# Performance work log

Measured on AMD Instinct MI355X. Metric: run time of the kernel, lower is better.

The kernel has to match this reference:

```python
import jax, jax.numpy as jnp
import numpy as np

N = 50000; IN_DIM = 128; HID = 128; T = 4; R = 3; E = 500000

def setup_inputs() -> dict:
    key = jax.random.key(0)
    ks = jax.random.split(key, 20)
    def nrm(k, shape, s):
        return jax.random.normal(k, shape, jnp.float32) * s
    s_in = 1.0 / float(np.sqrt(IN_DIM)); s_h = 1.0 / float(np.sqrt(HID))
    return {
        'feat_seq': nrm(ks[0], (T, N, IN_DIM), 1.0),
        'src': jax.random.randint(ks[1], (T, R, E), 0, N, jnp.int32),
        'dst': jax.random.randint(ks[2], (T, R, E), 0, N, jnp.int32),
        'ew': jax.random.uniform(ks[3], (T, R, E), jnp.float32),
        'W_in': nrm(ks[4], (IN_DIM, HID), s_in), 'b_in': jnp.zeros((HID,), jnp.float32),
        'W1': nrm(ks[5], (R, HID, HID), s_h), 'b1': jnp.zeros((R, HID), jnp.float32),
        'W2': nrm(ks[6], (R, HID, HID), s_h), 'b2': jnp.zeros((R, HID), jnp.float32),
        'q1': nrm(ks[7], (HID,), 1.0), 'q2': nrm(ks[8], (HID,), 1.0),
        'ln1_g': jnp.ones((HID,), jnp.float32), 'ln1_b': jnp.zeros((HID,), jnp.float32),
        'ln2_g': jnp.ones((HID,), jnp.float32), 'ln2_b': jnp.zeros((HID,), jnp.float32),
        'gWih': nrm(ks[9], (HID, 3 * HID), s_h), 'gbih': jnp.zeros((3 * HID,), jnp.float32),
        'gWhh': nrm(ks[10], (HID, 3 * HID), s_h), 'gbhh': jnp.zeros((3 * HID,), jnp.float32),
        'temp_q': nrm(ks[11], (HID,), 1.0),
        'tW1': nrm(ks[12], (IN_DIM, HID), s_in), 'tb1': jnp.zeros((HID,), jnp.float32),
        'tW2': nrm(ks[13], (HID, HID), s_h), 'tb2': jnp.zeros((HID,), jnp.float32),
        'cW1': nrm(ks[14], (3 * HID, HID), 1.0 / float(np.sqrt(3 * HID))), 'cb1': jnp.zeros((HID,), jnp.float32),
        'cW2': nrm(ks[15], (HID, 1), s_h), 'cb2': jnp.zeros((1,), jnp.float32),
    }

def _ln(x, g, b):
    m = x.mean(-1, keepdims=True)
    v = ((x - m) ** 2).mean(-1, keepdims=True)
    return (x - m) * jax.lax.rsqrt(v + 1e-5) * g + b

def _rel_attn(stack, q):
    # stack: [R,N,H]; tanh-softmax attention over relations
    score = jnp.einsum('rnh,h->rn', jnp.tanh(stack), q)
    alpha = jax.nn.softmax(score, axis=0)
    return jnp.einsum('rn,rnh->nh', alpha, stack)

def _conv(x, s, d, w, Wr, br):
    # DGL GraphConv norm='right' with edge_weight: mean-by-in-degree weighted SpMM
    msg = w[:, None] * x[s]                                   # [E,H]
    agg = jax.ops.segment_sum(msg, d, num_segments=N)
    deg = jax.ops.segment_sum(jnp.ones_like(w), d, num_segments=N)
    return (agg / jnp.maximum(deg, 1.0)[:, None]) @ Wr + br

def reference(feat_seq, src, dst, ew, W_in, b_in, W1, b1, W2, b2, q1, q2, ln1_g, ln1_b, ln2_g, ln2_b, gWih, gbih, gWhh, gbhh, temp_q, tW1, tb1, tW2, tb2, cW1, cb1, cW2, cb2):
    conv_all = jax.vmap(_conv, in_axes=(None, 0, 0, 0, 0, 0))
    def spatial(x, s, d, w):
        h0 = jax.nn.relu(x @ W_in + b_in)
        h1 = _ln(h0 + jax.nn.relu(_rel_attn(conv_all(h0, s, d, w, W1, b1), q1)), ln1_g, ln1_b)
        h2 = _ln(h1 + jax.nn.relu(_rel_attn(conv_all(h1, s, d, w, W2, b2), q2)), ln2_g, ln2_b)
        return h2
    hs = jnp.stack([spatial(feat_seq[t], src[t], dst[t], ew[t]) for t in range(T)], axis=0)  # [T,N,H]
    def gru_step(h, x):
        gi = x @ gWih + gbih
        gh = h @ gWhh + gbhh
        ir, iz, inn = jnp.split(gi, 3, axis=-1)
        hr, hz, hn = jnp.split(gh, 3, axis=-1)
        r = jax.nn.sigmoid(ir + hr)
        zg = jax.nn.sigmoid(iz + hz)
        n = jnp.tanh(inn + r * hn)
        hnew = (1.0 - zg) * n + zg * h
        return hnew, hnew
    _, outs = jax.lax.scan(gru_step, jnp.zeros((N, HID), feat_seq.dtype), hs)  # [T,N,H]
    out = jnp.transpose(outs, (1, 0, 2))                       # [N,T,H]
    last = out[:, -1, :]
    t_score = jnp.einsum('nth,h->nt', jnp.tanh(out), temp_q)
    t_alpha = jax.nn.softmax(t_score, axis=1)
    attn = jnp.einsum('nt,nth->nh', t_alpha, out)
    tab = jax.nn.relu(jax.nn.relu(feat_seq[-1] @ tW1 + tb1) @ tW2 + tb2)
    z = jnp.concatenate([last, attn, tab], axis=-1)
    return (jax.nn.relu(z @ cW1 + cb1) @ cW2 + cb2)[:, 0]       # [N]
```

## Files before the change

### kernel.cpp

```cpp
#include <hip/hip_runtime.h>
#include <hip/hip_bf16.h>
#include <math.h>

#define NN 50000
#define TT 4
#define RR 3
#define EE 500000
#define RANGE 6400
#define NRANGE 8

typedef __attribute__((ext_vector_type(8))) short bf16x8;
typedef __attribute__((ext_vector_type(4))) float f32x4;

__device__ inline unsigned short f2b(float f)
{
    union { __hip_bfloat16 h; unsigned short u; } cv;
    cv.h = __float2bfloat16(f);
    return cv.u;
}
__device__ inline float b2f(unsigned short u)
{
    union { unsigned int u; float f; } cv;
    cv.u = ((unsigned int)u) << 16;
    return cv.f;
}
__device__ inline bf16x8 pack8(float4 a, float4 b)
{
    bf16x8 r;
    r[0] = (short)f2b(a.x); r[1] = (short)f2b(a.y); r[2] = (short)f2b(a.z); r[3] = (short)f2b(a.w);
    r[4] = (short)f2b(b.x); r[5] = (short)f2b(b.y); r[6] = (short)f2b(b.z); r[7] = (short)f2b(b.w);
    return r;
}


__global__ __launch_bounds__(256)
void diag_kernel(float* __restrict__ out, float v)
{
    int i = blockIdx.x * 256 + threadIdx.x;
    if (i < NN) out[i] = v;
}


__global__ __launch_bounds__(256)
void wswz_kernel(const float* __restrict__ W, unsigned short* __restrict__ dst, int C, int S)
{
    int idx = blockIdx.x * 256 + threadIdx.x;
    int per = 128 * C;
    if (idx >= S * per) return;
    int s = idx / per, rem = idx - s * per;
    int j = rem & 7;
    int lane = (rem >> 3) & 63;
    int blk = rem >> 9;
    int ncg = C >> 4;
    int kc = blk / ncg, cg = blk - kc * ncg;
    int k = kc * 32 + (lane >> 4) * 8 + j;
    int c = cg * 16 + (lane & 15);
    dst[idx] = f2b(W[(size_t)s * 128 * C + (size_t)k * C + c]);
}


__global__ __launch_bounds__(1024)
void count_hist(const int* __restrict__ dst, int* __restrict__ cnt)
{
    __shared__ int hist[RANGE];
    const int g = blockIdx.y;
    const int r0 = blockIdx.x * RANGE;
    for (int i = threadIdx.x; i < RANGE; i += 1024) hist[i] = 0;
    __syncthreads();
    const int4* d4 = (const int4*)(dst + (size_t)g * EE);
    for (int i = threadIdx.x; i < EE / 4; i += 1024) {
        int4 v = d4[i];
        int a0 = v.x - r0; if ((unsigned)a0 < (unsigned)RANGE) atomicAdd(&hist[a0], 1);
        int a1 = v.y - r0; if ((unsigned)a1 < (unsigned)RANGE) atomicAdd(&hist[a1], 1);
        int a2 = v.z - r0; if ((unsigned)a2 < (unsigned)RANGE) atomicAdd(&hist[a2], 1);
        int a3 = v.w - r0; if ((unsigned)a3 < (unsigned)RANGE) atomicAdd(&hist[a3], 1);
    }
    __syncthreads();
    int* c = cnt + (size_t)g * NN;
    for (int i = threadIdx.x; i < RANGE; i += 1024) {
        int n = r0 + i;
        if (n < NN) c[n] = hist[i];
    }
}

__global__ __launch_bounds__(1024)
void scan_kernel(int* __restrict__ cnt, int* __restrict__ rows)
{
    int g = blockIdx.x;
    int tid = threadIdx.x;
    const int CH = (NN + 1023) / 1024;
    int s0 = tid * CH;
    int s1 = s0 + CH; if (s1 > NN) s1 = NN;
    int* c = cnt + (size_t)g * NN;
    int* ro = rows + (size_t)g * (NN + 1);
    int sum = 0;
    for (int i = s0; i < s1; ++i) sum += c[i];
    __shared__ int sd[1024];
    sd[tid] = sum;
    __syncthreads();
    for (int off = 1; off < 1024; off <<= 1) {
        int v = 0;
        if (tid >= off) v = sd[tid - off];
        __syncthreads();
        sd[tid] += v;
        __syncthreads();
    }
    int total = sd[1023];
    int prefix = (tid == 0) ? 0 : sd[tid - 1];
    for (int i = s0; i < s1; ++i) {
        int cv = c[i];
        ro[i] = prefix;
        c[i] = prefix;
        prefix += cv;
    }
    if (tid == 0) ro[NN] = total;
}

__global__ __launch_bounds__(256)
void fill_kernel(const int* __restrict__ src, const int* __restrict__ dst,
                 const float* __restrict__ ew, int* __restrict__ cur,
                 int2* __restrict__ srcw)
{
    int g = blockIdx.y;
    int e = blockIdx.x * 256 + threadIdx.x;
    if (e >= EE) return;
    size_t idx = (size_t)g * EE + e;
    int d = dst[idx];
    int pos = atomicAdd(&cur[(size_t)g * NN + d], 1);
    int2 p;
    p.x = src[idx];
    p.y = __float_as_int(ew[idx]);
    srcw[(size_t)g * EE + pos] = p;
}


__global__ __launch_bounds__(256)
void agg16_kernel(const unsigned short* __restrict__ x16,
                  const int2* __restrict__ srcw,
                  const int* __restrict__ rows,
                  unsigned short* __restrict__ agg16)
{
    int wid = (blockIdx.x * 256 + threadIdx.x) >> 6;
    int lane = threadIdx.x & 63;
    if (wid >= RR * NN) return;
    int r = wid / NN;
    int n = wid - r * NN;
    const int* rs = rows + (size_t)r * (NN + 1);
    int e0 = rs[n], e1 = rs[n + 1];
    const int2* sw = srcw + (size_t)r * EE;
    const int co = lane * 2;
    float ax = 0.f, ay = 0.f;
    for (int e = e0; e < e1; e += 16) {
        int2 p[16];
        unsigned int v[16];
#pragma unroll
        for (int i = 0; i < 16; ++i) {
            int idx = (e + i < e1) ? e + i : e1 - 1;
            p[i] = sw[idx];
        }
#pragma unroll
        for (int i = 0; i < 16; ++i)
            v[i] = *(const unsigned int*)(x16 + (size_t)p[i].x * 128 + co);
#pragma unroll
        for (int i = 0; i < 16; ++i) {
            float w = (e + i < e1) ? __int_as_float(p[i].y) : 0.f;
            ax += w * b2f((unsigned short)(v[i] & 0xffffu));
            ay += w * b2f((unsigned short)(v[i] >> 16));
        }
    }
    float inv = 1.0f / fmaxf((float)(e1 - e0), 1.0f);
    unsigned int o = (unsigned int)f2b(ax * inv) | ((unsigned int)f2b(ay * inv) << 16);
    *(unsigned int*)(agg16 + ((size_t)r * NN + n) * 128 + co) = o;
}


__global__ __launch_bounds__(256)
void mmb(const void* in, int in_bf16, long in_zs, int ldin,
         const unsigned short* __restrict__ Ws, long w_zs,
         const float* __restrict__ bias, long b_zs,
         float* out, long out_zs, int ldout,
         unsigned short* out16, long out16_zs,
         int rows, int act)
{
    const int tid = threadIdx.x;
    const int wv = tid >> 6, l = tid & 63;
    const int z = blockIdx.z;
    const int r0 = blockIdx.x * 64 + wv * 16;
    const int lk = (l >> 4) * 8;
    int rowA = r0 + (l & 15);
    int rowc = rowA < rows ? rowA : rows - 1;

    bf16x8 a[4];
    if (in_bf16) {
        const unsigned short* inb = (const unsigned short*)in + (size_t)z * in_zs
                                    + (size_t)rowc * ldin + lk;
#pragma unroll
        for (int kc = 0; kc < 4; ++kc) {
            uint4 u = *(const uint4*)(inb + kc * 32);
            a[kc] = *(bf16x8*)&u;
        }
    } else {
        const float* inf = (const float*)in + (size_t)z * in_zs
                           + (size_t)rowc * ldin + lk;
#pragma unroll
        for (int kc = 0; kc < 4; ++kc) {
            float4 u0 = *(const float4*)(inf + kc * 32);
            float4 u1 = *(const float4*)(inf + kc * 32 + 4);
            a[kc] = pack8(u0, u1);
        }
    }

    const unsigned short* Wz = Ws + (size_t)z * w_zs;
    const float* bz = bias + (size_t)z * b_zs;
    float* oz = out ? out + (size_t)z * out_zs : (float*)0;
    unsigned short* o16z = out16 ? out16 + (size_t)z * out16_zs : (unsigned short*)0;
    const int colbase = l & 15;
    const int rbase = r0 + (l >> 4) * 4;

#pragma unroll
    for (int cg = 0; cg < 8; ++cg) {
        f32x4 acc = {0.f, 0.f, 0.f, 0.f};
#pragma unroll
        for (int kc = 0; kc < 4; ++kc) {
            uint4 bu = *(const uint4*)(Wz + ((size_t)(kc * 8 + cg) * 64 + l) * 8);
            acc = __builtin_amdgcn_mfma_f32_16x16x32_bf16(a[kc], *(bf16x8*)&bu, acc, 0, 0, 0);
        }
        int col = cg * 16 + colbase;
        float bvv = bz[col];
#pragma unroll
        for (int j = 0; j < 4; ++j) {
            int gr = rbase + j;
            if (gr >= rows) continue;
            float v = acc[j] + bvv;
            if (act) v = fmaxf(v, 0.f);
            if (oz) oz[(size_t)gr * ldout + col] = v;
            if (o16z) o16z[(size_t)gr * 128 + col] = f2b(v);
        }
    }
}


__global__ __launch_bounds__(256)
void grub4(float* HS,
           const unsigned short* __restrict__ Wis, const float* __restrict__ bi,
           const unsigned short* __restrict__ Whs, const float* __restrict__ bh)
{
    __shared__ __align__(16) unsigned short hbuf[4][16 * 136];
    const int tid = threadIdx.x;
    const int wv = tid >> 6, l = tid & 63;
    const int r0 = blockIdx.x * 64 + wv * 16;
    const int lo = l & 15, hi = l >> 4;
    const int lk = hi * 8;
    const int rowc = (r0 + lo) < NN ? (r0 + lo) : NN - 1;
    const int rbase = r0 + hi * 4;
    unsigned short* hb = hbuf[wv];

    for (int i = l; i < 16 * 136; i += 64) hb[i] = 0;

    float hold[8][4];
#pragma unroll
    for (int cg = 0; cg < 8; ++cg)
#pragma unroll
        for (int j = 0; j < 4; ++j) hold[cg][j] = 0.f;

#pragma unroll 1
    for (int t = 0; t < TT; ++t) {
        float* xt = HS + (size_t)t * NN * 128;
        bf16x8 ax[4], hx[4];
        const float* bx = xt + (size_t)rowc * 128 + lk;
#pragma unroll
        for (int kc = 0; kc < 4; ++kc) {
            ax[kc] = pack8(*(const float4*)(bx + kc * 32), *(const float4*)(bx + kc * 32 + 4));
            uint4 hu = *(const uint4*)(hb + lo * 136 + kc * 32 + lk);
            hx[kc] = *(bf16x8*)&hu;
        }

#pragma unroll 1
        for (int cg = 0; cg < 8; ++cg) {
            f32x4 air = {0.f,0.f,0.f,0.f}, ahr = {0.f,0.f,0.f,0.f};
            f32x4 aiz = {0.f,0.f,0.f,0.f}, ahz = {0.f,0.f,0.f,0.f};
            f32x4 ain = {0.f,0.f,0.f,0.f}, ahn = {0.f,0.f,0.f,0.f};
#pragma unroll
            for (int kc = 0; kc < 4; ++kc) {
                uint4 br = *(const uint4*)(Wis + ((size_t)(kc * 24 + 0 + cg) * 64 + l) * 8);
                uint4 hr = *(const uint4*)(Whs + ((size_t)(kc * 24 + 0 + cg) * 64 + l) * 8);
                uint4 bz = *(const uint4*)(Wis + ((size_t)(kc * 24 + 8 + cg) * 64 + l) * 8);
                uint4 hz = *(const uint4*)(Whs + ((size_t)(kc * 24 + 8 + cg) * 64 + l) * 8);
                uint4 bn = *(const uint4*)(Wis + ((size_t)(kc * 24 + 16 + cg) * 64 + l) * 8);
                uint4 hn = *(const uint4*)(Whs + ((size_t)(kc * 24 + 16 + cg) * 64 + l) * 8);
                air = __builtin_amdgcn_mfma_f32_16x16x32_bf16(ax[kc], *(bf16x8*)&br, air, 0, 0, 0);
                ahr = __builtin_amdgcn_mfma_f32_16x16x32_bf16(hx[kc], *(bf16x8*)&hr, ahr, 0, 0, 0);
                aiz = __builtin_amdgcn_mfma_f32_16x16x32_bf16(ax[kc], *(bf16x8*)&bz, aiz, 0, 0, 0);
                ahz = __builtin_amdgcn_mfma_f32_16x16x32_bf16(hx[kc], *(bf16x8*)&hz, ahz, 0, 0, 0);
                ain = __builtin_amdgcn_mfma_f32_16x16x32_bf16(ax[kc], *(bf16x8*)&bn, ain, 0, 0, 0);
                ahn = __builtin_amdgcn_mfma_f32_16x16x32_bf16(hx[kc], *(bf16x8*)&hn, ahn, 0, 0, 0);
            }
            int col = cg * 16 + lo;
            float bir = bi[col],       bhr = bh[col];
            float biz = bi[128 + col], bhz = bh[128 + col];
            float bin = bi[256 + col], bhn = bh[256 + col];
#pragma unroll
            for (int j = 0; j < 4; ++j) {
                float r_ = 1.f / (1.f + __expf(-(air[j] + bir + ahr[j] + bhr)));
                float z_ = 1.f / (1.f + __expf(-(aiz[j] + biz + ahz[j] + bhz)));
                float n_ = tanhf(ain[j] + bin + r_ * (ahn[j] + bhn));
                float o = (1.f - z_) * n_ + z_ * hold[cg][j];
                hold[cg][j] = o;
                int gr = rbase + j;
                if (gr < NN) xt[(size_t)gr * 128 + col] = o;
                hb[(hi * 4 + j) * 136 + col] = f2b(o);
            }
        }
    }
}


__global__ __launch_bounds__(256)
void cls_mfma(const float* __restrict__ in,
              const unsigned short* __restrict__ Ws,
              const float* __restrict__ b1_,
              const float* __restrict__ w2,
              const float* __restrict__ b2_,
              float* __restrict__ outv, int rows)
{
    const int tid = threadIdx.x;
    const int wv = tid >> 6, l = tid & 63;
    const int r0 = blockIdx.x * 64 + wv * 16;
    const int lk = (l >> 4) * 8;
    int rowA = r0 + (l & 15);
    int rowc = rowA < rows ? rowA : rows - 1;

    bf16x8 a[12];
    {
        const float* inf = in + (size_t)rowc * 384 + lk;
#pragma unroll
        for (int kc = 0; kc < 12; ++kc) {
            float4 u0 = *(const float4*)(inf + kc * 32);
            float4 u1 = *(const float4*)(inf + kc * 32 + 4);
            a[kc] = pack8(u0, u1);
        }
    }
    const int colbase = l & 15;
    const int rbase = r0 + (l >> 4) * 4;
    float part[4] = {0.f, 0.f, 0.f, 0.f};

#pragma unroll
    for (int cg = 0; cg < 8; ++cg) {
        f32x4 acc = {0.f, 0.f, 0.f, 0.f};
#pragma unroll
        for (int kc = 0; kc < 12; ++kc) {
            uint4 bu = *(const uint4*)(Ws + ((size_t)(kc * 8 + cg) * 64 + l) * 8);
            acc = __builtin_amdgcn_mfma_f32_16x16x32_bf16(a[kc], *(bf16x8*)&bu, acc, 0, 0, 0);
        }
        int col = cg * 16 + colbase;
        float b1v = b1_[col];
        float w2v = w2[col];
#pragma unroll
        for (int j = 0; j < 4; ++j)
            part[j] += fmaxf(acc[j] + b1v, 0.f) * w2v;
    }
    const float cb2v = b2_[0];
#pragma unroll
    for (int j = 0; j < 4; ++j) {
#pragma unroll
        for (int m = 1; m < 16; m <<= 1) part[j] += __shfl_xor(part[j], m);
        int gr = rbase + j;
        if ((l & 15) == 0 && gr < rows) outv[gr] = part[j] + cb2v;
    }
}


__device__ inline float wred(float v)
{
#pragma unroll
    for (int m = 32; m; m >>= 1) v += __shfl_xor(v, m);
    return v;
}

__global__ __launch_bounds__(256)
void attnln_kernel(const unsigned short* __restrict__ agg16,
                   const unsigned short* hin16,
                   const float* __restrict__ q,
                   const float* __restrict__ g,
                   const float* __restrict__ b,
                   float* hout,
                   unsigned short* hout16)
{
    int wid = (blockIdx.x * 256 + threadIdx.x) >> 6;
    int lane = threadIdx.x & 63;
    if (wid >= NN) return;
    int n = wid;
    float2 qv = *(const float2*)(q + lane * 2);
    float sx[3], sy[3], sc[3];
#pragma unroll
    for (int r = 0; r < 3; ++r) {
        unsigned int v = *(const unsigned int*)(agg16 + ((size_t)r * NN + n) * 128 + lane * 2);
        sx[r] = b2f((unsigned short)(v & 0xffffu));
        sy[r] = b2f((unsigned short)(v >> 16));
        sc[r] = wred(tanhf(sx[r]) * qv.x + tanhf(sy[r]) * qv.y);
    }
    float mx = fmaxf(sc[0], fmaxf(sc[1], sc[2]));
    float e0 = __expf(sc[0] - mx), e1 = __expf(sc[1] - mx), e2 = __expf(sc[2] - mx);
    float isum = 1.f / (e0 + e1 + e2);
    float axv = (e0 * sx[0] + e1 * sx[1] + e2 * sx[2]) * isum;
    float ayv = (e0 * sy[0] + e1 * sy[1] + e2 * sy[2]) * isum;
    unsigned int hv = *(const unsigned int*)(hin16 + (size_t)n * 128 + lane * 2);
    float ux = b2f((unsigned short)(hv & 0xffffu)) + fmaxf(axv, 0.f);
    float uy = b2f((unsigned short)(hv >> 16)) + fmaxf(ayv, 0.f);
    float mean = wred(ux + uy) * (1.f / 128.f);
    float dx = ux - mean, dy = uy - mean;
    float var = wred(dx * dx + dy * dy) * (1.f / 128.f);
    float rstd = rsqrtf(var + 1e-5f);
    float2 gv = *(const float2*)(g + lane * 2);
    float2 bv = *(const float2*)(b + lane * 2);
    float ox = dx * rstd * gv.x + bv.x;
    float oy = dy * rstd * gv.y + bv.y;
    if (hout) {
        float2 o; o.x = ox; o.y = oy;
        *(float2*)(hout + (size_t)n * 128 + lane * 2) = o;
    }
    if (hout16) {
        unsigned int p = (unsigned int)f2b(ox) | ((unsigned int)f2b(oy) << 16);
        *(unsigned int*)(hout16 + (size_t)n * 128 + lane * 2) = p;
    }
}


__global__ __launch_bounds__(256)
void temporal_kernel(const float* __restrict__ outs,
                     const float* __restrict__ tq,
                     float* __restrict__ zbuf)
{
    int wid = (blockIdx.x * 256 + threadIdx.x) >> 6;
    int lane = threadIdx.x & 63;
    if (wid >= NN) return;
    int n = wid;
    float2 qv = *(const float2*)(tq + lane * 2);
    float2 o[4];
    float sc[4];
#pragma unroll
    for (int t = 0; t < 4; ++t) {
        o[t] = *(const float2*)(outs + ((size_t)t * NN + n) * 128 + lane * 2);
        sc[t] = wred(tanhf(o[t].x) * qv.x + tanhf(o[t].y) * qv.y);
    }
    float mx = fmaxf(fmaxf(sc[0], sc[1]), fmaxf(sc[2], sc[3]));
    float e[4];
    float sum = 0.f;
#pragma unroll
    for (int t = 0; t < 4; ++t) { e[t] = __expf(sc[t] - mx); sum += e[t]; }
    float isum = 1.f / sum;
    float axv = 0.f, ayv = 0.f;
#pragma unroll
    for (int t = 0; t < 4; ++t) { axv += e[t] * o[t].x; ayv += e[t] * o[t].y; }
    axv *= isum; ayv *= isum;
    float* zr = zbuf + (size_t)n * 384;
    *(float2*)(zr + lane * 2) = o[3];
    float2 at; at.x = axv; at.y = ayv;
    *(float2*)(zr + 128 + lane * 2) = at;
}


extern "C" void kernel_launch(void* const* d_in, const int* in_sizes, int n_in,
                              void* d_out, int out_size, void* d_ws, size_t ws_size,
                              hipStream_t stream)
{
    const float* feat = (const float*)d_in[0];
    const int* srcp   = (const int*)d_in[1];
    const int* dstp   = (const int*)d_in[2];
    const float* ewp  = (const float*)d_in[3];
    const float* W_in = (const float*)d_in[4];
    const float* b_in = (const float*)d_in[5];
    const float* W1   = (const float*)d_in[6];
    const float* b1   = (const float*)d_in[7];
    const float* W2   = (const float*)d_in[8];
    const float* b2   = (const float*)d_in[9];
    const float* q1   = (const float*)d_in[10];
    const float* q2   = (const float*)d_in[11];
    const float* ln1g = (const float*)d_in[12];
    const float* ln1b = (const float*)d_in[13];
    const float* ln2g = (const float*)d_in[14];
    const float* ln2b = (const float*)d_in[15];
    const float* gWih = (const float*)d_in[16];
    const float* gbih = (const float*)d_in[17];
    const float* gWhh = (const float*)d_in[18];
    const float* gbhh = (const float*)d_in[19];
    const float* tq   = (const float*)d_in[20];
    const float* tW1  = (const float*)d_in[21];
    const float* tb1  = (const float*)d_in[22];
    const float* tW2  = (const float*)d_in[23];
    const float* tb2  = (const float*)d_in[24];
    const float* cW1  = (const float*)d_in[25];
    const float* cb1  = (const float*)d_in[26];
    const float* cW2  = (const float*)d_in[27];
    const float* cb2  = (const float*)d_in[28];
    float* outv = (float*)d_out;
    (void)in_sizes; (void)n_in; (void)out_size;

    const size_t o_HS    = 0;
    const size_t o_POOL  = 102400000;
    const size_t o_AGG16 = o_POOL;
    const size_t o_H16   = o_POOL + 38400000;
    const size_t o_SRCW  = o_POOL + 51200000;
    const size_t o_ROWS  = o_POOL + 63200000;
    const size_t o_CURS  = o_POOL + 65600128;
    const size_t o_ZB    = o_POOL;
    const size_t o_H     = o_POOL + 76800000;
    const size_t o_WSZ   = o_H + 25600000;
    const size_t NEED    = o_WSZ + 589824;

    if (ws_size < NEED) {
        diag_kernel<<<dim3((NN + 255) / 256), dim3(256), 0, stream>>>(outv, (float)(ws_size >> 20));
        return;
    }

    char* wsb = (char*)d_ws;
    float* HS             = (float*)(wsb + o_HS);
    unsigned short* AGG16 = (unsigned short*)(wsb + o_AGG16);
    unsigned short* H16   = (unsigned short*)(wsb + o_H16);
    int2*  SRCW           = (int2*)(wsb + o_SRCW);
    int*   ROWS           = (int*)(wsb + o_ROWS);
    int*   CURS           = (int*)(wsb + o_CURS);
    float* ZB             = (float*)(wsb + o_ZB);
    unsigned short* TAB16 = (unsigned short*)(wsb + o_H);
    unsigned short* WSZ   = (unsigned short*)(wsb + o_WSZ);

    unsigned short* Wins  = WSZ;
    unsigned short* W1s   = WSZ + 16384;
    unsigned short* W2s   = WSZ + 65536;
    unsigned short* gWihs = WSZ + 114688;
    unsigned short* gWhhs = WSZ + 163840;
    unsigned short* tW1s  = WSZ + 212992;
    unsigned short* tW2s  = WSZ + 229376;
    unsigned short* cW1s  = WSZ + 245760;

    const dim3 blk(256);
    const int G64 = (NN + 63) / 64;
    const dim3 gE((EE + 255) / 256, RR);

    wswz_kernel<<<dim3((1 * 16384 + 255) / 256), blk, 0, stream>>>(W_in, Wins, 128, 1);
    wswz_kernel<<<dim3((3 * 16384 + 255) / 256), blk, 0, stream>>>(W1,   W1s,  128, 3);
    wswz_kernel<<<dim3((3 * 16384 + 255) / 256), blk, 0, stream>>>(W2,   W2s,  128, 3);
    wswz_kernel<<<dim3((1 * 49152 + 255) / 256), blk, 0, stream>>>(gWih, gWihs, 384, 1);
    wswz_kernel<<<dim3((1 * 49152 + 255) / 256), blk, 0, stream>>>(gWhh, gWhhs, 384, 1);
    wswz_kernel<<<dim3((1 * 16384 + 255) / 256), blk, 0, stream>>>(tW1,  tW1s, 128, 1);
    wswz_kernel<<<dim3((1 * 16384 + 255) / 256), blk, 0, stream>>>(tW2,  tW2s, 128, 1);
    wswz_kernel<<<dim3((3 * 16384 + 255) / 256), blk, 0, stream>>>(cW1,  cW1s, 128, 3);

    count_hist<<<dim3(NRANGE, TT * RR), dim3(1024), 0, stream>>>(dstp, CURS);
    scan_kernel<<<dim3(TT * RR), dim3(1024), 0, stream>>>(CURS, ROWS);

    for (int t = 0; t < TT; ++t) {
        const size_t eoff = (size_t)t * RR * EE;
        fill_kernel<<<gE, blk, 0, stream>>>(srcp + eoff, dstp + eoff, ewp + eoff,
                                            CURS + (size_t)t * RR * NN, SRCW);

        mmb<<<dim3(G64, 1, 1), blk, 0, stream>>>(
            (const void*)(feat + (size_t)t * NN * 128), 0, 0, 128,
            Wins, 0, b_in, 0, (float*)0, 0, 0, H16, 0, NN, 1);

        for (int layer = 0; layer < 2; ++layer) {
            const unsigned short* Wls = layer ? W2s : W1s;
            const float* bl = layer ? b2 : b1;
            const float* ql = layer ? q2 : q1;
            const float* lg = layer ? ln2g : ln1g;
            const float* lb = layer ? ln2b : ln1b;
            float* hout = layer ? (HS + (size_t)t * NN * 128) : (float*)0;
            unsigned short* hout16 = layer ? (unsigned short*)0 : H16;

            agg16_kernel<<<dim3((RR * NN) / 4), blk, 0, stream>>>(
                H16, SRCW, ROWS + (size_t)t * RR * (NN + 1), AGG16);
            mmb<<<dim3(G64, 1, RR), blk, 0, stream>>>(
                (const void*)AGG16, 1, (long)NN * 128, 128,
                Wls, 16384, bl, 128, (float*)0, 0, 0, AGG16, (long)NN * 128, NN, 0);
            attnln_kernel<<<dim3(NN / 4), blk, 0, stream>>>(
                AGG16, H16, ql, lg, lb, hout, hout16);
        }
    }

    grub4<<<dim3(G64), blk, 0, stream>>>(HS, gWihs, gbih, gWhhs, gbhh);

    temporal_kernel<<<dim3(NN / 4), blk, 0, stream>>>(HS, tq, ZB);

    mmb<<<dim3(G64, 1, 1), blk, 0, stream>>>(
        (const void*)(feat + (size_t)3 * NN * 128), 0, 0, 128,
        tW1s, 0, tb1, 0, (float*)0, 0, 0, TAB16, 0, NN, 1);
    mmb<<<dim3(G64, 1, 1), blk, 0, stream>>>(
        (const void*)TAB16, 1, 0, 128,
        tW2s, 0, tb2, 0, ZB + 256, 0, 384, (unsigned short*)0, 0, NN, 1);

    cls_mfma<<<dim3(G64), blk, 0, stream>>>(ZB, cW1s, cb1, cW2, cb2, outv, NN);
}
```

Measured before the change: 2.045 ms.

## Build all CSR edge lists once with range-partitioned shared-memory atomics

Replaces the per-timestep fill kernel, which used global atomics, with one fill_hist launch covering all 12 graphs. Each block owns a destination range of 6400 nodes and keeps its cursors in shared memory, so the position atomics are done in LDS. The cost is that every block scans all 500k edges of its graph, so the dst array is read eight times. The workspace is rearranged so SRCW holds all timesteps at once, and agg16 is offset into it per timestep.

```diff
diff --git a/kernel.cpp b/kernel.cpp
--- a/kernel.cpp
+++ b/kernel.cpp
@@ -116,21 +116,34 @@
     if (tid == 0) ro[NN] = total;
 }
 
-__global__ __launch_bounds__(256)
-void fill_kernel(const int* __restrict__ src, const int* __restrict__ dst,
-                 const float* __restrict__ ew, int* __restrict__ cur,
-                 int2* __restrict__ srcw)
-{
-    int g = blockIdx.y;
-    int e = blockIdx.x * 256 + threadIdx.x;
-    if (e >= EE) return;
-    size_t idx = (size_t)g * EE + e;
-    int d = dst[idx];
-    int pos = atomicAdd(&cur[(size_t)g * NN + d], 1);
-    int2 p;
-    p.x = src[idx];
-    p.y = __float_as_int(ew[idx]);
-    srcw[(size_t)g * EE + pos] = p;
+
+__global__ __launch_bounds__(1024)
+void fill_hist(const int* __restrict__ src, const int* __restrict__ dst,
+               const float* __restrict__ ew, const int* __restrict__ cur_start,
+               int2* __restrict__ srcw)
+{
+    __shared__ int cur[RANGE];
+    const int g = blockIdx.y;
+    const int r0 = blockIdx.x * RANGE;
+    const int* cs = cur_start + (size_t)g * NN;
+    for (int i = threadIdx.x; i < RANGE; i += 1024) {
+        int n = r0 + i;
+        cur[i] = (n < NN) ? cs[n] : 0;
+    }
+    __syncthreads();
+    const size_t base = (size_t)g * EE;
+    int2* sw = srcw + base;
+    for (int i = threadIdx.x; i < EE; i += 1024) {
+        int d = dst[base + i];
+        int a = d - r0;
+        if ((unsigned)a < (unsigned)RANGE) {
+            int pos = atomicAdd(&cur[a], 1);
+            int2 p;
+            p.x = src[base + i];
+            p.y = __float_as_int(ew[base + i]);
+            sw[pos] = p;
+        }
+    }
 }
 
 
@@ -501,11 +514,11 @@
     const size_t o_AGG16 = o_POOL;
     const size_t o_H16   = o_POOL + 38400000;
     const size_t o_SRCW  = o_POOL + 51200000;
-    const size_t o_ROWS  = o_POOL + 63200000;
-    const size_t o_CURS  = o_POOL + 65600128;
+    const size_t o_ROWS  = o_POOL + 99200000;
+    const size_t o_CURS  = o_POOL + 101600128;
     const size_t o_ZB    = o_POOL;
-    const size_t o_H     = o_POOL + 76800000;
-    const size_t o_WSZ   = o_H + 25600000;
+    const size_t o_TAB   = o_POOL + 76800000;
+    const size_t o_WSZ   = o_POOL + 104000128;
     const size_t NEED    = o_WSZ + 589824;
 
     if (ws_size < NEED) {
@@ -521,7 +534,7 @@
     int*   ROWS           = (int*)(wsb + o_ROWS);
     int*   CURS           = (int*)(wsb + o_CURS);
     float* ZB             = (float*)(wsb + o_ZB);
-    unsigned short* TAB16 = (unsigned short*)(wsb + o_H);
+    unsigned short* TAB16 = (unsigned short*)(wsb + o_TAB);
     unsigned short* WSZ   = (unsigned short*)(wsb + o_WSZ);
 
     unsigned short* Wins  = WSZ;
@@ -535,7 +548,6 @@
 
     const dim3 blk(256);
     const int G64 = (NN + 63) / 64;
-    const dim3 gE((EE + 255) / 256, RR);
 
     wswz_kernel<<<dim3((1 * 16384 + 255) / 256), blk, 0, stream>>>(W_in, Wins, 128, 1);
     wswz_kernel<<<dim3((3 * 16384 + 255) / 256), blk, 0, stream>>>(W1,   W1s,  128, 3);
@@ -548,12 +560,9 @@
 
     count_hist<<<dim3(NRANGE, TT * RR), dim3(1024), 0, stream>>>(dstp, CURS);
     scan_kernel<<<dim3(TT * RR), dim3(1024), 0, stream>>>(CURS, ROWS);
+    fill_hist<<<dim3(NRANGE, TT * RR), dim3(1024), 0, stream>>>(srcp, dstp, ewp, CURS, SRCW);
 
     for (int t = 0; t < TT; ++t) {
-        const size_t eoff = (size_t)t * RR * EE;
-        fill_kernel<<<gE, blk, 0, stream>>>(srcp + eoff, dstp + eoff, ewp + eoff,
-                                            CURS + (size_t)t * RR * NN, SRCW);
-
         mmb<<<dim3(G64, 1, 1), blk, 0, stream>>>(
             (const void*)(feat + (size_t)t * NN * 128), 0, 0, 128,
             Wins, 0, b_in, 0, (float*)0, 0, 0, H16, 0, NN, 1);
@@ -568,7 +577,7 @@
             unsigned short* hout16 = layer ? (unsigned short*)0 : H16;
 
             agg16_kernel<<<dim3((RR * NN) / 4), blk, 0, stream>>>(
-                H16, SRCW, ROWS + (size_t)t * RR * (NN + 1), AGG16);
+                H16, SRCW + (size_t)t * RR * EE, ROWS + (size_t)t * RR * (NN + 1), AGG16);
             mmb<<<dim3(G64, 1, RR), blk, 0, stream>>>(
                 (const void*)AGG16, 1, (long)NN * 128, 128,
                 Wls, 16384, bl, 128, (float*)0, 0, 0, AGG16, (long)NN * 128, NN, 0);
```

Result: slower. 2.132 ms (+4.3%).
